# Optimization experiments

Measured on AMD Instinct MI355X. Metric: run time of the kernel, lower is better.

## Reference

```python
import jax, jax.numpy as jnp
import numpy as np

IN_FEATURES = 4096
OUT_FEATURES = 11008
TOKENS = 32


def ternarize_weight(w):
    # abs-mean scale, clamped; threshold at 0.7*abs_mean
    abs_mean = jnp.maximum(jnp.mean(jnp.abs(w)), 1e-5)
    threshold = 0.7 * abs_mean
    q = jnp.where(w > threshold, 1.0, jnp.where(w < -threshold, -1.0, 0.0))
    # straight-through estimator: forward value q*abs_mean, grad passes to w
    return w + jax.lax.stop_gradient(q * abs_mean - w)


def setup_inputs() -> dict:
    key = jax.random.key(0)
    kx, kw = jax.random.split(key)
    x = jax.random.normal(kx, (TOKENS, IN_FEATURES), dtype=jnp.float32)
    # master fp32 weights, init std = 1/sqrt(in_features) as in the module
    weight = jax.random.normal(kw, (OUT_FEATURES, IN_FEATURES), dtype=jnp.float32) / np.sqrt(IN_FEATURES)
    return {"x": x, "weight": weight}


def reference(x, weight):
    # ternary_active=True, ternary_alpha=1.0 path: fully ternarized weights
    w_q = ternarize_weight(weight)
    # F.linear(x, w): [T, in] @ [out, in]^T -> [T, out]
    return jnp.einsum('ti,oi->to', x, w_q)
```

## Files before the change

kernel.cpp:

```cpp
#include <hip/hip_runtime.h>
#include <hip/hip_bf16.h>
#include <stdint.h>

#define IN_F 4096
#define OUT_F 11008
#define TOKENS 32
#define NELEM_W (OUT_F * IN_F)

typedef __attribute__((ext_vector_type(8))) __bf16 bf16x8;
typedef __attribute__((ext_vector_type(4))) float  f32x4;

__device__ __forceinline__ uint32_t bfr(float v) {
    uint32_t u = __float_as_uint(v);
    uint32_t r = u + 0x7FFFu + ((u >> 16) & 1u);
    return r >> 16;
}

#define ABSUM_BLOCKS 2048
#define XCVT_BLOCKS  64

__global__ __launch_bounds__(256) void absum_xcvt_kernel(const float* __restrict__ w,
                                                         const float* __restrict__ x,
                                                         double* __restrict__ ws_sum,
                                                         uint4* __restrict__ xb) {
    if (blockIdx.x >= ABSUM_BLOCKS) {
        int i = (blockIdx.x - ABSUM_BLOCKS) * 256 + threadIdx.x;
        const float4* x4 = (const float4*)x;
        float4 a0 = x4[i * 2];
        float4 a1 = x4[i * 2 + 1];
        uint4 o;
        o.x = bfr(a0.x) | (bfr(a0.y) << 16);
        o.y = bfr(a0.z) | (bfr(a0.w) << 16);
        o.z = bfr(a1.x) | (bfr(a1.y) << 16);
        o.w = bfr(a1.z) | (bfr(a1.w) << 16);
        xb[i] = o;
        return;
    }
    int tid = blockIdx.x * blockDim.x + threadIdx.x;
    int stride = ABSUM_BLOCKS * 256;
    const float4* w4 = (const float4*)w;
    const int n4 = NELEM_W / 4;
    float s = 0.f;
    for (int i = tid; i < n4; i += stride) {
        float4 v = w4[i];
        s += fabsf(v.x) + fabsf(v.y) + fabsf(v.z) + fabsf(v.w);
    }
    for (int off = 32; off > 0; off >>= 1)
        s += __shfl_down(s, off, 64);
    __shared__ float wsum[4];
    int lane = threadIdx.x & 63;
    int wv   = threadIdx.x >> 6;
    if (lane == 0) wsum[wv] = s;
    __syncthreads();
    if (threadIdx.x == 0) {
        float t = wsum[0] + wsum[1] + wsum[2] + wsum[3];
        atomicAdd(ws_sum, (double)t);
    }
}

__global__ void finalize_kernel(double* __restrict__ ws) {
    double mean = ws[0] / (double)NELEM_W;
    if (mean < 1e-5) mean = 1e-5;
    float mf = (float)mean;
    float* f = (float*)ws;
    f[2] = 0.7f * mf;
    f[3] = mf;
}

__device__ __forceinline__ uint32_t tern1(float v, float thr) {
    uint32_t u  = __float_as_uint(v);
    uint32_t pm = (u & 0x80000000u) | 0x3F800000u;
    return (__builtin_fabsf(v) > thr) ? pm : 0u;
}

__device__ __forceinline__ uint2 tern4(float4 b, float thr) {
    uint32_t q0 = tern1(b.x, thr), q1 = tern1(b.y, thr);
    uint32_t q2 = tern1(b.z, thr), q3 = tern1(b.w, thr);
    uint2 r;
    r.x = (q0 >> 16) | (q1 & 0xFFFF0000u);
    r.y = (q2 >> 16) | (q3 & 0xFFFF0000u);
    return r;
}

#define CHUNKS 8
#define WAVE_LDS 2304
#define SMEM_BYTES 9216

__global__ __launch_bounds__(256, 3) void ternary_gemm(const float* __restrict__ w,
                                                       const float* __restrict__ wsf,
                                                       const __bf16* __restrict__ xb,
                                                       float* __restrict__ out) {
    __shared__ char smem_raw[SMEM_BYTES];
    const float thr   = wsf[2];
    const float scale = wsf[3];
    const int og   = blockIdx.x >> 1;
    const int kh   = blockIdx.x & 1;
    const int tid  = threadIdx.x;
    const int wv   = tid >> 6;
    const int lane = tid & 63;
    const int col  = lane & 15;
    const int quad = lane >> 4;
    const int rlan = lane & 15;

    const int kw = kh * 2048 + wv * 512;

    const float* wp = w + (size_t)(og * 16 + quad) * IN_F + kw + rlan * 4;
    char* stage = smem_raw + wv * WAVE_LDS;
    char* wr    = stage + quad * 144 + rlan * 8;
    const char* rd = stage + col * 144;
    const __bf16* xq = xb + (size_t)col * IN_F + kw + quad * 8;

    f32x4 acc0 = {0.f, 0.f, 0.f, 0.f};
    f32x4 acc1 = {0.f, 0.f, 0.f, 0.f};

    float4 w0 = *(const float4*)(wp);
    float4 w1 = *(const float4*)(wp + 4 * IN_F);
    float4 w2 = *(const float4*)(wp + 8 * IN_F);
    float4 w3 = *(const float4*)(wp + 12 * IN_F);
    bf16x8 a00 = *(const bf16x8*)(xq);
    bf16x8 a01 = *(const bf16x8*)(xq + 32);
    bf16x8 a10 = *(const bf16x8*)(xq + 16 * IN_F);
    bf16x8 a11 = *(const bf16x8*)(xq + 16 * IN_F + 32);

#pragma unroll 2
    for (int c = 0; c < CHUNKS; ++c) {
        uint2 t0 = tern4(w0, thr);
        uint2 t1 = tern4(w1, thr);
        uint2 t2 = tern4(w2, thr);
        uint2 t3 = tern4(w3, thr);
        *(uint2*)(wr)        = t0;
        *(uint2*)(wr + 576)  = t1;
        *(uint2*)(wr + 1152) = t2;
        *(uint2*)(wr + 1728) = t3;

        bf16x8 n00 = a00, n01 = a01, n10 = a10, n11 = a11;
        if (c + 1 < CHUNKS) {
            const float*  np = wp + (c + 1) * 64;
            const __bf16* xn = xq + (c + 1) * 64;
            w0  = *(const float4*)(np);
            w1  = *(const float4*)(np + 4 * IN_F);
            w2  = *(const float4*)(np + 8 * IN_F);
            w3  = *(const float4*)(np + 12 * IN_F);
            n00 = *(const bf16x8*)(xn);
            n01 = *(const bf16x8*)(xn + 32);
            n10 = *(const bf16x8*)(xn + 16 * IN_F);
            n11 = *(const bf16x8*)(xn + 16 * IN_F + 32);
        }

        bf16x8 bw0 = *(const bf16x8*)(rd + quad * 16);
        bf16x8 bw1 = *(const bf16x8*)(rd + 64 + quad * 16);
        acc0 = __builtin_amdgcn_mfma_f32_16x16x32_bf16(a00, bw0, acc0, 0, 0, 0);
        acc1 = __builtin_amdgcn_mfma_f32_16x16x32_bf16(a10, bw0, acc1, 0, 0, 0);
        acc0 = __builtin_amdgcn_mfma_f32_16x16x32_bf16(a01, bw1, acc0, 0, 0, 0);
        acc1 = __builtin_amdgcn_mfma_f32_16x16x32_bf16(a11, bw1, acc1, 0, 0, 0);

        a00 = n00; a01 = n01; a10 = n10; a11 = n11;
    }

    __syncthreads();
    float* red  = (float*)smem_raw;
    float* base = red + wv * 512;
#pragma unroll
    for (int r = 0; r < 4; ++r) base[r * 64 + lane]       = acc0[r];
#pragma unroll
    for (int r = 0; r < 4; ++r) base[256 + r * 64 + lane] = acc1[r];
    __syncthreads();

#pragma unroll
    for (int p = tid; p < 512; p += 256) {
        int t = p >> 4, cc = p & 15;
        int a = t >> 4;
        int q = (t >> 2) & 3;
        int r = t & 3;
        int idx = a * 256 + r * 64 + q * 16 + cc;
        float s = red[idx] + red[512 + idx] + red[1024 + idx] + red[1536 + idx];
        atomicAdd(out + (size_t)t * OUT_F + og * 16 + cc, s * scale);
    }
}

extern "C" void kernel_launch(void* const* d_in, const int* in_sizes, int n_in,
                              void* d_out, int out_size, void* d_ws, size_t ws_size,
                              hipStream_t stream) {
    const float* x = (const float*)d_in[0];
    const float* w = (const float*)d_in[1];
    float* out     = (float*)d_out;
    double* wsd    = (double*)d_ws;
    uint4* xb      = (uint4*)((char*)d_ws + 64);

    hipMemsetAsync(d_ws, 0, 16, stream);
    hipMemsetAsync(d_out, 0, sizeof(float) * TOKENS * OUT_F, stream);

    absum_xcvt_kernel<<<ABSUM_BLOCKS + XCVT_BLOCKS, 256, 0, stream>>>(w, x, wsd, xb);
    finalize_kernel<<<1, 1, 0, stream>>>(wsd);
    ternary_gemm<<<(OUT_F / 16) * 2, 256, 0, stream>>>(w, (const float*)d_ws,
                                                       (const __bf16*)((char*)d_ws + 64), out);
}
```

Baseline: 293.0 us.

## Replace atomics with partial buffers, shrink GEMM blocks, deepen prefetch

Drops both memsets and the double atomic reduction: each abs-sum block now writes its own partial, and a 256-thread finalize kernel reduces them. The GEMM moves to 128-thread blocks with 16 chunks per wave and a two-deep register prefetch. It writes per-K-half partials to a workspace instead of issuing atomicAdds, and a new combine kernel sums the two halves and applies the scale. Ternary packing now uses v_perm. This trades the memsets and atomic traffic for an extra kernel launch and a 2.8MB round trip through the partial buffer.

```diff
diff --git a/kernel.cpp b/kernel.cpp
--- a/kernel.cpp
+++ b/kernel.cpp
@@ -6,9 +6,14 @@
 #define OUT_F 11008
 #define TOKENS 32
 #define NELEM_W (OUT_F * IN_F)
+#define OUT_ELEMS (TOKENS * OUT_F)
 
 typedef __attribute__((ext_vector_type(8))) __bf16 bf16x8;
 typedef __attribute__((ext_vector_type(4))) float  f32x4;
+
+#define XB_OFF    64
+#define GPART_OFF 262208
+#define APART_OFF 3080256
 
 __device__ __forceinline__ uint32_t bfr(float v) {
     uint32_t u = __float_as_uint(v);
@@ -21,7 +26,7 @@
 
 __global__ __launch_bounds__(256) void absum_xcvt_kernel(const float* __restrict__ w,
                                                          const float* __restrict__ x,
-                                                         double* __restrict__ ws_sum,
+                                                         float* __restrict__ apart,
                                                          uint4* __restrict__ xb) {
     if (blockIdx.x >= ABSUM_BLOCKS) {
         int i = (blockIdx.x - ABSUM_BLOCKS) * 256 + threadIdx.x;
@@ -52,19 +57,30 @@
     int wv   = threadIdx.x >> 6;
     if (lane == 0) wsum[wv] = s;
     __syncthreads();
+    if (threadIdx.x == 0)
+        apart[blockIdx.x] = wsum[0] + wsum[1] + wsum[2] + wsum[3];
+}
+
+__global__ __launch_bounds__(256) void finalize_kernel(const float* __restrict__ apart,
+                                                       float* __restrict__ wsf) {
+    float s = 0.f;
+#pragma unroll
+    for (int j = 0; j < 8; ++j)
+        s += apart[threadIdx.x + 256 * j];
+    for (int off = 32; off > 0; off >>= 1)
+        s += __shfl_down(s, off, 64);
+    __shared__ float wsum[4];
+    int lane = threadIdx.x & 63;
+    int wv   = threadIdx.x >> 6;
+    if (lane == 0) wsum[wv] = s;
+    __syncthreads();
     if (threadIdx.x == 0) {
-        float t = wsum[0] + wsum[1] + wsum[2] + wsum[3];
-        atomicAdd(ws_sum, (double)t);
-    }
-}
-
-__global__ void finalize_kernel(double* __restrict__ ws) {
-    double mean = ws[0] / (double)NELEM_W;
-    if (mean < 1e-5) mean = 1e-5;
-    float mf = (float)mean;
-    float* f = (float*)ws;
-    f[2] = 0.7f * mf;
-    f[3] = mf;
+        double mean = (double)(wsum[0] + wsum[1] + wsum[2] + wsum[3]) / (double)NELEM_W;
+        if (mean < 1e-5) mean = 1e-5;
+        float mf = (float)mean;
+        wsf[2] = 0.7f * mf;
+        wsf[3] = mf;
+    }
 }
 
 __device__ __forceinline__ uint32_t tern1(float v, float thr) {
@@ -77,22 +93,21 @@
     uint32_t q0 = tern1(b.x, thr), q1 = tern1(b.y, thr);
     uint32_t q2 = tern1(b.z, thr), q3 = tern1(b.w, thr);
     uint2 r;
-    r.x = (q0 >> 16) | (q1 & 0xFFFF0000u);
-    r.y = (q2 >> 16) | (q3 & 0xFFFF0000u);
+    r.x = __builtin_amdgcn_perm(q1, q0, 0x07060302u);
+    r.y = __builtin_amdgcn_perm(q3, q2, 0x07060302u);
     return r;
 }
 
-#define CHUNKS 8
+#define CHUNKS 16
 #define WAVE_LDS 2304
-#define SMEM_BYTES 9216
-
-__global__ __launch_bounds__(256, 3) void ternary_gemm(const float* __restrict__ w,
+#define SMEM_BYTES 4608
+
+__global__ __launch_bounds__(128, 4) void ternary_gemm(const float* __restrict__ w,
                                                        const float* __restrict__ wsf,
                                                        const __bf16* __restrict__ xb,
-                                                       float* __restrict__ out) {
+                                                       float* __restrict__ gpart) {
     __shared__ char smem_raw[SMEM_BYTES];
-    const float thr   = wsf[2];
-    const float scale = wsf[3];
+    const float thr = wsf[2];
     const int og   = blockIdx.x >> 1;
     const int kh   = blockIdx.x & 1;
     const int tid  = threadIdx.x;
@@ -102,7 +117,7 @@
     const int quad = lane >> 4;
     const int rlan = lane & 15;
 
-    const int kw = kh * 2048 + wv * 512;
+    const int kw = kh * 2048 + wv * 1024;
 
     const float* wp = w + (size_t)(og * 16 + quad) * IN_F + kw + rlan * 4;
     char* stage = smem_raw + wv * WAVE_LDS;
@@ -113,49 +128,60 @@
     f32x4 acc0 = {0.f, 0.f, 0.f, 0.f};
     f32x4 acc1 = {0.f, 0.f, 0.f, 0.f};
 
-    float4 w0 = *(const float4*)(wp);
-    float4 w1 = *(const float4*)(wp + 4 * IN_F);
-    float4 w2 = *(const float4*)(wp + 8 * IN_F);
-    float4 w3 = *(const float4*)(wp + 12 * IN_F);
-    bf16x8 a00 = *(const bf16x8*)(xq);
-    bf16x8 a01 = *(const bf16x8*)(xq + 32);
-    bf16x8 a10 = *(const bf16x8*)(xq + 16 * IN_F);
-    bf16x8 a11 = *(const bf16x8*)(xq + 16 * IN_F + 32);
-
-#pragma unroll 2
-    for (int c = 0; c < CHUNKS; ++c) {
-        uint2 t0 = tern4(w0, thr);
-        uint2 t1 = tern4(w1, thr);
-        uint2 t2 = tern4(w2, thr);
-        uint2 t3 = tern4(w3, thr);
-        *(uint2*)(wr)        = t0;
-        *(uint2*)(wr + 576)  = t1;
-        *(uint2*)(wr + 1152) = t2;
-        *(uint2*)(wr + 1728) = t3;
-
-        bf16x8 n00 = a00, n01 = a01, n10 = a10, n11 = a11;
-        if (c + 1 < CHUNKS) {
-            const float*  np = wp + (c + 1) * 64;
-            const __bf16* xn = xq + (c + 1) * 64;
-            w0  = *(const float4*)(np);
-            w1  = *(const float4*)(np + 4 * IN_F);
-            w2  = *(const float4*)(np + 8 * IN_F);
-            w3  = *(const float4*)(np + 12 * IN_F);
-            n00 = *(const bf16x8*)(xn);
-            n01 = *(const bf16x8*)(xn + 32);
-            n10 = *(const bf16x8*)(xn + 16 * IN_F);
-            n11 = *(const bf16x8*)(xn + 16 * IN_F + 32);
-        }
-
-        bf16x8 bw0 = *(const bf16x8*)(rd + quad * 16);
-        bf16x8 bw1 = *(const bf16x8*)(rd + 64 + quad * 16);
-        acc0 = __builtin_amdgcn_mfma_f32_16x16x32_bf16(a00, bw0, acc0, 0, 0, 0);
-        acc1 = __builtin_amdgcn_mfma_f32_16x16x32_bf16(a10, bw0, acc1, 0, 0, 0);
-        acc0 = __builtin_amdgcn_mfma_f32_16x16x32_bf16(a01, bw1, acc0, 0, 0, 0);
-        acc1 = __builtin_amdgcn_mfma_f32_16x16x32_bf16(a11, bw1, acc1, 0, 0, 0);
-
-        a00 = n00; a01 = n01; a10 = n10; a11 = n11;
-    }
+    float4 wb[2][4];
+    bf16x8 xv[2][4];
+
+#pragma unroll
+    for (int c = 0; c < 2; ++c) {
+        const float*  np = wp + c * 64;
+        const __bf16* xn = xq + c * 64;
+        wb[c][0] = *(const float4*)(np);
+        wb[c][1] = *(const float4*)(np + 4 * IN_F);
+        wb[c][2] = *(const float4*)(np + 8 * IN_F);
+        wb[c][3] = *(const float4*)(np + 12 * IN_F);
+        xv[c][0] = *(const bf16x8*)(xn);
+        xv[c][1] = *(const bf16x8*)(xn + 32);
+        xv[c][2] = *(const bf16x8*)(xn + 16 * IN_F);
+        xv[c][3] = *(const bf16x8*)(xn + 16 * IN_F + 32);
+    }
+
+#define GEMM_BODY(c, cur)                                                      \
+    {                                                                          \
+        uint2 t0 = tern4(wb[cur][0], thr);                                     \
+        uint2 t1 = tern4(wb[cur][1], thr);                                     \
+        uint2 t2 = tern4(wb[cur][2], thr);                                     \
+        uint2 t3 = tern4(wb[cur][3], thr);                                     \
+        *(uint2*)(wr)        = t0;                                             \
+        *(uint2*)(wr + 576)  = t1;                                             \
+        *(uint2*)(wr + 1152) = t2;                                             \
+        *(uint2*)(wr + 1728) = t3;                                             \
+        bf16x8 a00 = xv[cur][0], a01 = xv[cur][1];                             \
+        bf16x8 a10 = xv[cur][2], a11 = xv[cur][3];                             \
+        if ((c) + 2 < CHUNKS) {                                                \
+            const float*  np = wp + ((c) + 2) * 64;                            \
+            const __bf16* xn = xq + ((c) + 2) * 64;                            \
+            wb[cur][0] = *(const float4*)(np);                                 \
+            wb[cur][1] = *(const float4*)(np + 4 * IN_F);                      \
+            wb[cur][2] = *(const float4*)(np + 8 * IN_F);                      \
+            wb[cur][3] = *(const float4*)(np + 12 * IN_F);                     \
+            xv[cur][0] = *(const bf16x8*)(xn);                                 \
+            xv[cur][1] = *(const bf16x8*)(xn + 32);                            \
+            xv[cur][2] = *(const bf16x8*)(xn + 16 * IN_F);                     \
+            xv[cur][3] = *(const bf16x8*)(xn + 16 * IN_F + 32);                \
+        }                                                                      \
+        bf16x8 bw0 = *(const bf16x8*)(rd + quad * 16);                         \
+        bf16x8 bw1 = *(const bf16x8*)(rd + 64 + quad * 16);                    \
+        acc0 = __builtin_amdgcn_mfma_f32_16x16x32_bf16(a00, bw0, acc0, 0, 0, 0); \
+        acc1 = __builtin_amdgcn_mfma_f32_16x16x32_bf16(a10, bw0, acc1, 0, 0, 0); \
+        acc0 = __builtin_amdgcn_mfma_f32_16x16x32_bf16(a01, bw1, acc0, 0, 0, 0); \
+        acc1 = __builtin_amdgcn_mfma_f32_16x16x32_bf16(a11, bw1, acc1, 0, 0, 0); \
+    }
+
+    for (int c = 0; c < CHUNKS; c += 2) {
+        GEMM_BODY(c, 0)
+        GEMM_BODY(c + 1, 1)
+    }
+#undef GEMM_BODY
 
     __syncthreads();
     float* red  = (float*)smem_raw;
@@ -166,16 +192,31 @@
     for (int r = 0; r < 4; ++r) base[256 + r * 64 + lane] = acc1[r];
     __syncthreads();
 
-#pragma unroll
-    for (int p = tid; p < 512; p += 256) {
+    float* gp = gpart + (size_t)kh * OUT_ELEMS;
+    for (int p = tid; p < 512; p += 128) {
         int t = p >> 4, cc = p & 15;
         int a = t >> 4;
         int q = (t >> 2) & 3;
         int r = t & 3;
         int idx = a * 256 + r * 64 + q * 16 + cc;
-        float s = red[idx] + red[512 + idx] + red[1024 + idx] + red[1536 + idx];
-        atomicAdd(out + (size_t)t * OUT_F + og * 16 + cc, s * scale);
-    }
+        gp[(size_t)t * OUT_F + og * 16 + cc] = red[idx] + red[512 + idx];
+    }
+}
+
+__global__ __launch_bounds__(256) void combine_kernel(const float* __restrict__ gpart,
+                                                      const float* __restrict__ wsf,
+                                                      float* __restrict__ out) {
+    const float sc = wsf[3];
+    int i = blockIdx.x * 256 + threadIdx.x;
+    const float4* p0 = (const float4*)gpart;
+    const float4* p1 = (const float4*)(gpart + OUT_ELEMS);
+    float4 a = p0[i], b = p1[i];
+    float4 o;
+    o.x = (a.x + b.x) * sc;
+    o.y = (a.y + b.y) * sc;
+    o.z = (a.z + b.z) * sc;
+    o.w = (a.w + b.w) * sc;
+    ((float4*)out)[i] = o;
 }
 
 extern "C" void kernel_launch(void* const* d_in, const int* in_sizes, int n_in,
@@ -184,14 +225,15 @@
     const float* x = (const float*)d_in[0];
     const float* w = (const float*)d_in[1];
     float* out     = (float*)d_out;
-    double* wsd    = (double*)d_ws;
-    uint4* xb      = (uint4*)((char*)d_ws + 64);
-
-    hipMemsetAsync(d_ws, 0, 16, stream);
-    hipMemsetAsync(d_out, 0, sizeof(float) * TOKENS * OUT_F, stream);
-
-    absum_xcvt_kernel<<<ABSUM_BLOCKS + XCVT_BLOCKS, 256, 0, stream>>>(w, x, wsd, xb);
-    finalize_kernel<<<1, 1, 0, stream>>>(wsd);
-    ternary_gemm<<<(OUT_F / 16) * 2, 256, 0, stream>>>(w, (const float*)d_ws,
-                                                       (const __bf16*)((char*)d_ws + 64), out);
-}
+    char* ws       = (char*)d_ws;
+
+    float* wsf     = (float*)ws;
+    uint4* xb      = (uint4*)(ws + XB_OFF);
+    float* gpart   = (float*)(ws + GPART_OFF);
+    float* apart   = (float*)(ws + APART_OFF);
+
+    absum_xcvt_kernel<<<ABSUM_BLOCKS + XCVT_BLOCKS, 256, 0, stream>>>(w, x, apart, xb);
+    finalize_kernel<<<1, 256, 0, stream>>>(apart, wsf);
+    ternary_gemm<<<(OUT_F / 16) * 2, 128, 0, stream>>>(w, wsf, (const __bf16*)(ws + XB_OFF), gpart);
+    combine_kernel<<<OUT_ELEMS / 4 / 256, 256, 0, stream>>>(gpart, wsf, out);
+}
```

Result: faster. 279.4 us (-4.6%).
